# Kernel tuning notes

Hardware: AMD Instinct MI355X
Metric: run time of the kernel (lower is better)

The kernel has to match this reference:

```python
import jax, jax.numpy as jnp
import numpy as np

D = 512      # word_embedding_dim (dim_in == dim_out)
HEADS = 8    # isab_num_heads
M = 16       # isab_num_inds
B = 2048     # batch_news_num = batch_size * news_num
S = 32       # max_title_length
EPS = 1e-5   # torch LayerNorm default eps


def _layer_norm(x, g, b):
    mu = jnp.mean(x, axis=-1, keepdims=True)
    var = jnp.mean((x - mu) ** 2, axis=-1, keepdims=True)
    return (x - mu) * jax.lax.rsqrt(var + EPS) * g + b


def _mab(Qin, Kin, Wqkv, bqkv, Wo, bo, g0, b0, g1, b1):
    # Faithful to torch MAB: linear Q/K/V, head split via reshape (equivalent
    # to split/cat since cat-back restores head slices), scale by sqrt(dim_V).
    d = Wqkv.shape[-1]
    Q = Qin @ Wqkv[0] + bqkv[0]          # [B, Sq, d]
    K = Kin @ Wqkv[1] + bqkv[1]          # [B, Sk, d]
    V = Kin @ Wqkv[2] + bqkv[2]
    Bn, Sq, _ = Q.shape
    Sk = K.shape[1]
    hd = d // HEADS
    Qh = Q.reshape(Bn, Sq, HEADS, hd)
    Kh = K.reshape(Bn, Sk, HEADS, hd)
    Vh = V.reshape(Bn, Sk, HEADS, hd)
    scores = jnp.einsum('bqhd,bkhd->bhqk', Qh, Kh) / jnp.sqrt(jnp.asarray(d, Q.dtype))
    A = jax.nn.softmax(scores, axis=-1)
    Oh = Qh + jnp.einsum('bhqk,bkhd->bqhd', A, Vh)   # residual on Q_
    O = Oh.reshape(Bn, Sq, d)
    O = _layer_norm(O, g0, b0)                        # ln0
    O = O + jax.nn.relu(O @ Wo + bo)                  # O + relu(fc_o(O))
    O = _layer_norm(O, g1, b1)                        # ln1
    return O


def _isab(X, I, p0, p1):
    Iq = jnp.broadcast_to(I, (X.shape[0],) + I.shape[1:])  # I.repeat(B,1,1)
    Hm = _mab(Iq, X, *p0)   # mab0(I, X) -> [B, M, d]
    return _mab(X, Hm, *p1)  # mab1(X, H) -> [B, S, d]


def setup_inputs() -> dict:
    key = jax.random.key(0)
    ks = jax.random.split(key, 12)
    sc = 1.0 / np.sqrt(D)
    inp = {
        'x': jax.random.normal(ks[0], (B, S, D), dtype=jnp.float32),
        'I': jax.random.normal(ks[1], (1, M, D), dtype=jnp.float32) * sc,
        'mab0_Wqkv': jax.random.normal(ks[2], (3, D, D), dtype=jnp.float32) * sc,
        'mab0_bqkv': jnp.zeros((3, D), dtype=jnp.float32),
        'mab0_Wo': jax.random.normal(ks[3], (D, D), dtype=jnp.float32) * sc,
        'mab0_bo': jnp.zeros((D,), dtype=jnp.float32),
        'mab0_g0': jnp.ones((D,), dtype=jnp.float32),
        'mab0_b0': jnp.zeros((D,), dtype=jnp.float32),
        'mab0_g1': jnp.ones((D,), dtype=jnp.float32),
        'mab0_b1': jnp.zeros((D,), dtype=jnp.float32),
        'mab1_Wqkv': jax.random.normal(ks[4], (3, D, D), dtype=jnp.float32) * sc,
        'mab1_bqkv': jnp.zeros((3, D), dtype=jnp.float32),
        'mab1_Wo': jax.random.normal(ks[5], (D, D), dtype=jnp.float32) * sc,
        'mab1_bo': jnp.zeros((D,), dtype=jnp.float32),
        'mab1_g0': jnp.ones((D,), dtype=jnp.float32),
        'mab1_b0': jnp.zeros((D,), dtype=jnp.float32),
        'mab1_g1': jnp.ones((D,), dtype=jnp.float32),
        'mab1_b1': jnp.zeros((D,), dtype=jnp.float32),
    }
    return inp


def reference(x, I,
              mab0_Wqkv, mab0_bqkv, mab0_Wo, mab0_bo, mab0_g0, mab0_b0, mab0_g1, mab0_b1,
              mab1_Wqkv, mab1_bqkv, mab1_Wo, mab1_bo, mab1_g0, mab1_b0, mab1_g1, mab1_b1):
    p0 = (mab0_Wqkv, mab0_bqkv, mab0_Wo, mab0_bo, mab0_g0, mab0_b0, mab0_g1, mab0_b1)
    p1 = (mab1_Wqkv, mab1_bqkv, mab1_Wo, mab1_bo, mab1_g0, mab1_b0, mab1_g1, mab1_b1)
    # CIDER title path (eval mode, dropout=identity): ISAB applied twice, mean pool
    h1 = _isab(x, I, p0, p1)
    h2 = _isab(h1, I, p0, p1)
    return jnp.mean(h2, axis=1)   # [B, D] title_embedding
```

## Files before the change

kernel.cpp:

```cpp
#include <hip/hip_runtime.h>
#include <hip/hip_bf16.h>

#define D 512
#define BATCH 2048
#define SEQ 32
#define MIND 16

typedef __hip_bfloat16 bf16;
typedef __attribute__((ext_vector_type(8))) short s8v;
typedef __attribute__((ext_vector_type(4))) short s4v;
typedef __attribute__((ext_vector_type(4))) float f4v;

#define SWZ(row, kb) (((row) << 10) + ((kb) ^ (((row) & 7) << 4)))

__device__ __forceinline__ ushort f2bu(float f) {
    bf16 h = __float2bfloat16(f); ushort u; __builtin_memcpy(&u, &h, 2); return u;
}
__device__ __forceinline__ float bu2f(ushort u) {
    unsigned x = ((unsigned)u) << 16; float f; __builtin_memcpy(&f, &x, 4); return f;
}

__device__ __forceinline__ float wave_sum(float v) {
#pragma unroll
    for (int off = 32; off >= 1; off >>= 1) v += __shfl_xor(v, off, 64);
    return v;
}

struct WPtrs { const float* s[7]; };

__global__ __launch_bounds__(256) void wtrans7(WPtrs wp, ushort* __restrict__ Wt) {
    const float* W = wp.s[blockIdx.z];
    ushort* dst = Wt + (size_t)blockIdx.z * 262144;
    __shared__ float t[32][33];
    const int k0 = blockIdx.x * 32, n0 = blockIdx.y * 32;
    const int lx = threadIdx.x & 31, ly = threadIdx.x >> 5;
    for (int i = ly; i < 32; i += 8) t[i][lx] = W[(size_t)(k0 + i) * D + n0 + lx];
    __syncthreads();
    for (int i = ly; i < 32; i += 8)
        dst[(size_t)(n0 + i) * D + k0 + lx] = f2bu(t[lx][i]);
}

__global__ __launch_bounds__(256) void q0_kernel(
    const float* __restrict__ I, const float* __restrict__ Wq,
    const float* __restrict__ bq, ushort* __restrict__ Q0b)
{
    const int q = blockIdx.x;
    const int c = threadIdx.x;
    float a0 = 0.f, a1 = 0.f;
    for (int k = 0; k < D; ++k) {
        const float iv = I[q * D + k];
        a0 = fmaf(iv, Wq[(size_t)k * D + c], a0);
        a1 = fmaf(iv, Wq[(size_t)k * D + c + 256], a1);
    }
    Q0b[q * D + c]       = f2bu(a0 + bq[c]);
    Q0b[q * D + c + 256] = f2bu(a1 + bq[c + 256]);
}

__global__ __launch_bounds__(256) void conv_bf16(const float* __restrict__ x,
                                                 ushort* __restrict__ xb, long n4) {
    for (long i = (long)blockIdx.x * 256 + threadIdx.x; i < n4; i += (long)gridDim.x * 256) {
        const float4 v = ((const float4*)x)[i];
        s4v o = {(short)f2bu(v.x), (short)f2bu(v.y), (short)f2bu(v.z), (short)f2bu(v.w)};
        ((s4v*)xb)[i] = o;
    }
}

template <bool RESFUSE, bool LNA>
__global__ __launch_bounds__(512, 4) void gemm512(
    const ushort* __restrict__ Ab, const ushort* __restrict__ Wt,
    const float* __restrict__ bias,
    const float* __restrict__ lng, const float* __restrict__ lnb,
    ushort* __restrict__ Cb)
{
    __shared__ __align__(16) char sA[64 * 1024];
    const int tid = threadIdx.x, lane = tid & 63, wv = tid >> 6;
    const size_t m0 = (size_t)blockIdx.x * 64;

    for (int c = tid; c < 64 * 128; c += 512) {
        const int row = c >> 7, k4 = (c & 127) << 2;
        *(s4v*)(sA + SWZ(row, k4 * 2)) = *(const s4v*)(Ab + (m0 + row) * D + k4);
    }
    __syncthreads();

    if constexpr (LNA) {
        for (int i = wv; i < 64; i += 8) {
            float v[8];
#pragma unroll
            for (int j = 0; j < 8; ++j)
                v[j] = bu2f(*(const ushort*)(sA + SWZ(i, 2 * (lane + 64 * j))));
            float s = 0.f;
#pragma unroll
            for (int j = 0; j < 8; ++j) s += v[j];
            s = wave_sum(s);
            const float mu = s * (1.f / 512.f);
            float q2 = 0.f;
#pragma unroll
            for (int j = 0; j < 8; ++j) { const float t = v[j] - mu; q2 = fmaf(t, t, q2); }
            q2 = wave_sum(q2);
            const float inv = rsqrtf(q2 * (1.f / 512.f) + 1e-5f);
#pragma unroll
            for (int j = 0; j < 8; ++j) {
                const int d0 = lane + 64 * j;
                *(ushort*)(sA + SWZ(i, 2 * d0)) = f2bu((v[j] - mu) * inv * lng[d0] + lnb[d0]);
            }
        }
        __syncthreads();
    }

    constexpr int RT = 4;
    f4v acc[RT][4];
#pragma unroll
    for (int i = 0; i < RT; ++i)
#pragma unroll
        for (int j = 0; j < 4; ++j) acc[i][j] = (f4v){0.f, 0.f, 0.f, 0.f};
    const int m = lane & 15, g = lane >> 4;
    const int swm = (m & 7) << 4;
    const ushort* Bp = Wt + ((size_t)(wv * 64 + m) << 9) + 8 * g;

#pragma unroll
    for (int k0 = 0; k0 < 512; k0 += 32) {
        s8v bfr[4];
#pragma unroll
        for (int ct = 0; ct < 4; ++ct) bfr[ct] = *(const s8v*)(Bp + ct * 8192 + k0);
        const int kb = 2 * (k0 + 8 * g);
        s8v a[RT];
#pragma unroll
        for (int rt = 0; rt < RT; ++rt)
            a[rt] = *(const s8v*)(sA + ((rt * 16 + m) << 10) + (kb ^ swm));
#pragma unroll
        for (int ct = 0; ct < 4; ++ct)
#pragma unroll
            for (int rt = 0; rt < RT; ++rt)
                acc[rt][ct] = __builtin_amdgcn_mfma_f32_16x16x32_bf16(a[rt], bfr[ct], acc[rt][ct], 0, 0, 0);
    }

#pragma unroll
    for (int ct = 0; ct < 4; ++ct) {
        const int col = wv * 64 + ct * 16 + m;
        const float bb = bias[col];
#pragma unroll
        for (int rt = 0; rt < RT; ++rt)
#pragma unroll
            for (int r = 0; r < 4; ++r) {
                const int row = rt * 16 + g * 4 + r;
                float v = acc[rt][ct][r] + bb;
                if (RESFUSE)
                    v = bu2f(*(const ushort*)(sA + SWZ(row, 2 * col))) + fmaxf(v, 0.f);
                Cb[(m0 + row) * D + col] = f2bu(v);
            }
    }
}

template <int SQ, int SK, bool QSHARED>
__global__ __launch_bounds__(64) void attn_core(
    const ushort* __restrict__ Qb, const ushort* __restrict__ Kb,
    const ushort* __restrict__ Vb, ushort* __restrict__ Ob)
{
    constexpr int RS = 72;
    __shared__ __align__(16) ushort sQ[SQ * RS];
    __shared__ __align__(16) ushort sK[SK * RS];
    __shared__ __align__(16) ushort sV[SK * RS];
    __shared__ float sS[SQ][SK + 1];

    const int lane = threadIdx.x;
    const int b = blockIdx.x, h = blockIdx.y;
    const size_t qbase = (QSHARED ? (size_t)0 : (size_t)b * SQ * D) + h * 64;
    const size_t kbase = (size_t)b * SK * D + h * 64;

    for (int idx = lane; idx < SQ * 16; idx += 64) {
        const int r = idx >> 4, c4 = (idx & 15) << 2;
        *(s4v*)(sQ + r * RS + c4) = *(const s4v*)(Qb + qbase + (size_t)r * D + c4);
    }
    for (int idx = lane; idx < SK * 16; idx += 64) {
        const int r = idx >> 4, c4 = (idx & 15) << 2;
        *(s4v*)(sK + r * RS + c4) = *(const s4v*)(Kb + kbase + (size_t)r * D + c4);
        *(s4v*)(sV + r * RS + c4) = *(const s4v*)(Vb + kbase + (size_t)r * D + c4);
    }
    __syncthreads();

    const float scale = 0.044194173824159216f;
#pragma unroll
    for (int o = 0; o < SQ * SK / 64; ++o) {
        const int idx = o * 64 + lane;
        const int q = idx / SK, k = idx % SK;
        float s = 0.f;
#pragma unroll
        for (int dd = 0; dd < 64; dd += 8) {
            const s8v aq = *(const s8v*)(sQ + q * RS + dd);
            const s8v ak = *(const s8v*)(sK + k * RS + dd);
#pragma unroll
            for (int e = 0; e < 8; ++e)
                s = fmaf(bu2f((ushort)aq[e]), bu2f((ushort)ak[e]), s);
        }
        sS[q][k] = s * scale;
    }
    __syncthreads();

    if (lane < SQ) {
        float* row = sS[lane];
        float mx = row[0];
#pragma unroll
        for (int k = 1; k < SK; ++k) mx = fmaxf(mx, row[k]);
        float sum = 0.f;
#pragma unroll
        for (int k = 0; k < SK; ++k) { const float e = __expf(row[k] - mx); row[k] = e; sum += e; }
        const float inv = 1.f / sum;
#pragma unroll
        for (int k = 0; k < SK; ++k) row[k] *= inv;
    }
    __syncthreads();

    float acc[SQ];
#pragma unroll
    for (int q = 0; q < SQ; ++q) acc[q] = 0.f;
#pragma unroll 4
    for (int k = 0; k < SK; ++k) {
        const float v = bu2f(sV[k * RS + lane]);
#pragma unroll
        for (int q = 0; q < SQ; ++q) acc[q] = fmaf(sS[q][k], v, acc[q]);
    }
    const size_t obase = (size_t)b * SQ * D + h * 64 + lane;
#pragma unroll
    for (int q = 0; q < SQ; ++q)
        Ob[obase + (size_t)q * D] = f2bu(bu2f(sQ[q * RS + lane]) + acc[q]);
}

__global__ __launch_bounds__(512) void ln_meanpool(
    const ushort* __restrict__ U, const float* __restrict__ gg,
    const float* __restrict__ bb, float* __restrict__ outp)
{
    __shared__ float sP[8][512];
    const int tid = threadIdx.x, lane = tid & 63, wv = tid >> 6;
    const size_t b = blockIdx.x;
    float a[8];
#pragma unroll
    for (int j = 0; j < 8; ++j) a[j] = 0.f;
    for (int i = wv; i < 32; i += 8) {
        const ushort* u = U + ((size_t)b * 32 + i) * D;
        float v[8];
#pragma unroll
        for (int j = 0; j < 8; ++j) v[j] = bu2f(u[lane + 64 * j]);
        float s = 0.f;
#pragma unroll
        for (int j = 0; j < 8; ++j) s += v[j];
        s = wave_sum(s);
        const float mu = s * (1.f / 512.f);
        float q2 = 0.f;
#pragma unroll
        for (int j = 0; j < 8; ++j) { const float t = v[j] - mu; q2 = fmaf(t, t, q2); }
        q2 = wave_sum(q2);
        const float inv = rsqrtf(q2 * (1.f / 512.f) + 1e-5f);
#pragma unroll
        for (int j = 0; j < 8; ++j) {
            const int d0 = lane + 64 * j;
            a[j] += (v[j] - mu) * inv * gg[d0] + bb[d0];
        }
    }
#pragma unroll
    for (int j = 0; j < 8; ++j) sP[wv][lane + 64 * j] = a[j];
    __syncthreads();
    float s = 0.f;
#pragma unroll
    for (int w = 0; w < 8; ++w) s += sP[w][tid];
    outp[b * D + tid] = s * (1.f / 32.f);
}

extern "C" void kernel_launch(void* const* d_in, const int* in_sizes, int n_in,
                              void* d_out, int out_size, void* d_ws, size_t ws_size,
                              hipStream_t stream) {
    (void)in_sizes; (void)n_in; (void)out_size; (void)ws_size;

    const float* x     = (const float*)d_in[0];
    const float* I     = (const float*)d_in[1];
    const float* W0    = (const float*)d_in[2];
    const float* bqkv0 = (const float*)d_in[3];
    const float* Wo0   = (const float*)d_in[4];
    const float* bo0   = (const float*)d_in[5];
    const float* g00   = (const float*)d_in[6];
    const float* b00   = (const float*)d_in[7];
    const float* g01   = (const float*)d_in[8];
    const float* b01   = (const float*)d_in[9];
    const float* W1    = (const float*)d_in[10];
    const float* bqkv1 = (const float*)d_in[11];
    const float* Wo1   = (const float*)d_in[12];
    const float* bo1   = (const float*)d_in[13];
    const float* g10   = (const float*)d_in[14];
    const float* b10   = (const float*)d_in[15];
    const float* g11   = (const float*)d_in[16];
    const float* b11   = (const float*)d_in[17];

    const float* Wq0 = W0;     const float* Wk0 = W0 + D * D;  const float* Wv0 = W0 + 2 * D * D;
    const float* bq0 = bqkv0;  const float* bk0 = bqkv0 + D;   const float* bv0 = bqkv0 + 2 * D;
    const float* Wq1 = W1;     const float* Wk1 = W1 + D * D;  const float* Wv1 = W1 + 2 * D * D;
    const float* bq1 = bqkv1;  const float* bk1 = bqkv1 + D;   const float* bv1 = bqkv1 + 2 * D;

    char* ws = (char*)d_ws;
    ushort* Q0b = (ushort*)ws;
    ushort* Wt  = (ushort*)(ws + 32768);
    char* base = ws + 32768 + 7 * 524288;
    ushort* P0 = (ushort*)(base);
    ushort* P1 = (ushort*)(base + ((size_t)64 << 20));
    ushort* P2 = (ushort*)(base + ((size_t)128 << 20));
    ushort* P3 = (ushort*)(base + ((size_t)192 << 20));
    const size_t HALF = (size_t)16 << 20;
    ushort* P0hi = P0 + HALF;
    ushort* P1hi = P1 + HALF;
    ushort* P3hi = P3 + HALF;

    ushort* WtK0 = Wt + 0 * 262144;
    ushort* WtV0 = Wt + 1 * 262144;
    ushort* WtO0 = Wt + 2 * 262144;
    ushort* WtQ1 = Wt + 3 * 262144;
    ushort* WtK1 = Wt + 4 * 262144;
    ushort* WtV1 = Wt + 5 * 262144;
    ushort* WtO1 = Wt + 6 * 262144;

    WPtrs wp; wp.s[0] = Wk0; wp.s[1] = Wv0; wp.s[2] = Wo0; wp.s[3] = Wq1;
    wp.s[4] = Wk1; wp.s[5] = Wv1; wp.s[6] = Wo1;
    wtrans7<<<dim3(16, 16, 7), 256, 0, stream>>>(wp, Wt);
    q0_kernel<<<MIND, 256, 0, stream>>>(I, Wq0, bq0, Q0b);
    conv_bf16<<<4096, 256, 0, stream>>>(x, P0, (long)BATCH * SEQ * D / 4);

    constexpr int GBS = BATCH * SEQ / 64;
    constexpr int GBM = BATCH * MIND / 64;
    const dim3 ag(BATCH, 8);

    gemm512<false, false><<<GBS, 512, 0, stream>>>(P0, WtK0, bk0, g00, b00, P1);
    gemm512<false, false><<<GBS, 512, 0, stream>>>(P0, WtV0, bv0, g00, b00, P2);
    attn_core<MIND, SEQ, true><<<ag, 64, 0, stream>>>(Q0b, P1, P2, P3);
    gemm512<true, true><<<GBM, 512, 0, stream>>>(P3, WtO0, bo0, g00, b00, P3hi);
    gemm512<false, true><<<GBM, 512, 0, stream>>>(P3hi, WtK1, bk1, g01, b01, P1);
    gemm512<false, true><<<GBM, 512, 0, stream>>>(P3hi, WtV1, bv1, g01, b01, P1hi);
    gemm512<false, false><<<GBS, 512, 0, stream>>>(P0, WtQ1, bq1, g00, b00, P2);
    attn_core<SEQ, MIND, false><<<ag, 64, 0, stream>>>(P2, P1, P1hi, P0);
    gemm512<true, true><<<GBS, 512, 0, stream>>>(P0, WtO1, bo1, g10, b10, P3);

    gemm512<false, true><<<GBS, 512, 0, stream>>>(P3, WtK0, bk0, g11, b11, P1);
    gemm512<false, true><<<GBS, 512, 0, stream>>>(P3, WtV0, bv0, g11, b11, P2);
    attn_core<MIND, SEQ, true><<<ag, 64, 0, stream>>>(Q0b, P1, P2, P0);
    gemm512<true, true><<<GBM, 512, 0, stream>>>(P0, WtO0, bo0, g00, b00, P0hi);
    gemm512<false, true><<<GBM, 512, 0, stream>>>(P0hi, WtK1, bk1, g01, b01, P1);
    gemm512<false, true><<<GBM, 512, 0, stream>>>(P0hi, WtV1, bv1, g01, b01, P1hi);
    gemm512<false, true><<<GBS, 512, 0, stream>>>(P3, WtQ1, bq1, g11, b11, P2);
    attn_core<SEQ, MIND, false><<<ag, 64, 0, stream>>>(P2, P1, P1hi, P3);
    gemm512<true, true><<<GBS, 512, 0, stream>>>(P3, WtO1, bo1, g10, b10, P0);

    ln_meanpool<<<BATCH, 512, 0, stream>>>(P0, g11, b11, (float*)d_out);
}
```

Measured before the change: 1.502 ms.

## Fuse K/V/Q projections into one multi-output GEMM with staged coalesced stores

Replaces the single-output gemm512 with a templated gemmN that loads the A tile once and computes up to three projections (K, V, Q) against it, cutting repeated A loads and kernel launches. Epilogue results are staged through a swizzled shared buffer so global stores become 16-byte row writes instead of scattered 2-byte writes. The attention output is written in place with a strided layout, and a SPARSEA row remap lets the next GEMM read it directly, which shrinks the buffer set. The cost is extra shared memory and extra barriers in the epilogue, which may lower occupancy.

```diff
diff --git a/kernel.cpp b/kernel.cpp
--- a/kernel.cpp
+++ b/kernel.cpp
@@ -65,20 +65,24 @@
     }
 }
 
-template <bool RESFUSE, bool LNA>
-__global__ __launch_bounds__(512, 4) void gemm512(
-    const ushort* __restrict__ Ab, const ushort* __restrict__ Wt,
-    const float* __restrict__ bias,
-    const float* __restrict__ lng, const float* __restrict__ lnb,
-    ushort* __restrict__ Cb)
+template <int NOUT, bool RESFUSE, bool LNA, bool SPARSEA>
+__global__ __launch_bounds__(512, 4) void gemmN(
+    const ushort* __restrict__ Ab,
+    const ushort* __restrict__ Wt0, const float* __restrict__ bias0, ushort* __restrict__ C0,
+    const ushort* __restrict__ Wt1, const float* __restrict__ bias1, ushort* __restrict__ C1,
+    const ushort* __restrict__ Wt2, const float* __restrict__ bias2, ushort* __restrict__ C2,
+    const float* __restrict__ lng, const float* __restrict__ lnb)
 {
     __shared__ __align__(16) char sA[64 * 1024];
+    __shared__ __align__(16) char sC[16 * 1024];
     const int tid = threadIdx.x, lane = tid & 63, wv = tid >> 6;
     const size_t m0 = (size_t)blockIdx.x * 64;
 
-    for (int c = tid; c < 64 * 128; c += 512) {
-        const int row = c >> 7, k4 = (c & 127) << 2;
-        *(s4v*)(sA + SWZ(row, k4 * 2)) = *(const s4v*)(Ab + (m0 + row) * D + k4);
+    for (int c = tid; c < 64 * 64; c += 512) {
+        const int row = c >> 6, k8 = (c & 63) << 3;
+        const size_t L = m0 + row;
+        const size_t pr = SPARSEA ? ((L >> 4) * 32 + (L & 15)) : L;
+        *(s8v*)(sA + SWZ(row, k8 * 2)) = *(const s8v*)(Ab + pr * D + k8);
     }
     __syncthreads();
 
@@ -107,51 +111,67 @@
         __syncthreads();
     }
 
-    constexpr int RT = 4;
-    f4v acc[RT][4];
-#pragma unroll
-    for (int i = 0; i < RT; ++i)
-#pragma unroll
-        for (int j = 0; j < 4; ++j) acc[i][j] = (f4v){0.f, 0.f, 0.f, 0.f};
     const int m = lane & 15, g = lane >> 4;
     const int swm = (m & 7) << 4;
-    const ushort* Bp = Wt + ((size_t)(wv * 64 + m) << 9) + 8 * g;
-
-#pragma unroll
-    for (int k0 = 0; k0 < 512; k0 += 32) {
-        s8v bfr[4];
-#pragma unroll
-        for (int ct = 0; ct < 4; ++ct) bfr[ct] = *(const s8v*)(Bp + ct * 8192 + k0);
-        const int kb = 2 * (k0 + 8 * g);
-        s8v a[RT];
-#pragma unroll
-        for (int rt = 0; rt < RT; ++rt)
-            a[rt] = *(const s8v*)(sA + ((rt * 16 + m) << 10) + (kb ^ swm));
-#pragma unroll
-        for (int ct = 0; ct < 4; ++ct)
-#pragma unroll
-            for (int rt = 0; rt < RT; ++rt)
-                acc[rt][ct] = __builtin_amdgcn_mfma_f32_16x16x32_bf16(a[rt], bfr[ct], acc[rt][ct], 0, 0, 0);
-    }
-
-#pragma unroll
-    for (int ct = 0; ct < 4; ++ct) {
-        const int col = wv * 64 + ct * 16 + m;
-        const float bb = bias[col];
-#pragma unroll
-        for (int rt = 0; rt < RT; ++rt)
-#pragma unroll
-            for (int r = 0; r < 4; ++r) {
-                const int row = rt * 16 + g * 4 + r;
-                float v = acc[rt][ct][r] + bb;
-                if (RESFUSE)
-                    v = bu2f(*(const ushort*)(sA + SWZ(row, 2 * col))) + fmaxf(v, 0.f);
-                Cb[(m0 + row) * D + col] = f2bu(v);
+    const ushort* Wts[3]  = {Wt0, Wt1, Wt2};
+    const float*  bias[3] = {bias0, bias1, bias2};
+    ushort*       Cs[3]   = {C0, C1, C2};
+
+#pragma unroll
+    for (int o = 0; o < NOUT; ++o) {
+        const ushort* Bp = Wts[o] + ((size_t)(wv * 64 + m) << 9) + 8 * g;
+        f4v acc[4][4];
+#pragma unroll
+        for (int i = 0; i < 4; ++i)
+#pragma unroll
+            for (int j = 0; j < 4; ++j) acc[i][j] = (f4v){0.f, 0.f, 0.f, 0.f};
+
+#pragma unroll
+        for (int k0 = 0; k0 < 512; k0 += 32) {
+            s8v bfr[4];
+#pragma unroll
+            for (int ct = 0; ct < 4; ++ct) bfr[ct] = *(const s8v*)(Bp + ct * 8192 + k0);
+            const int kb = 2 * (k0 + 8 * g);
+            s8v a[4];
+#pragma unroll
+            for (int rt = 0; rt < 4; ++rt)
+                a[rt] = *(const s8v*)(sA + ((rt * 16 + m) << 10) + (kb ^ swm));
+#pragma unroll
+            for (int ct = 0; ct < 4; ++ct)
+#pragma unroll
+                for (int rt = 0; rt < 4; ++rt)
+                    acc[rt][ct] = __builtin_amdgcn_mfma_f32_16x16x32_bf16(a[rt], bfr[ct], acc[rt][ct], 0, 0, 0);
+        }
+
+        ushort* Cb = Cs[o];
+        const float* bb = bias[o];
+#pragma unroll 1
+        for (int rt = 0; rt < 4; ++rt) {
+            __syncthreads();
+#pragma unroll
+            for (int ct = 0; ct < 4; ++ct) {
+                const int col = wv * 64 + ct * 16 + m;
+                const float bv = bb[col];
+#pragma unroll
+                for (int r = 0; r < 4; ++r) {
+                    const int lrow = g * 4 + r;
+                    float v = acc[rt][ct][r] + bv;
+                    if (RESFUSE)
+                        v = bu2f(*(const ushort*)(sA + SWZ(rt * 16 + lrow, 2 * col))) + fmaxf(v, 0.f);
+                    *(ushort*)(sC + SWZ(lrow, 2 * col)) = f2bu(v);
+                }
             }
-    }
-}
-
-template <int SQ, int SK, bool QSHARED>
+            __syncthreads();
+            for (int c = tid; c < 16 * 64; c += 512) {
+                const int row = c >> 6, k8 = (c & 63) << 3;
+                *(s8v*)(Cb + (m0 + rt * 16 + row) * D + k8) = *(const s8v*)(sC + SWZ(row, k8 * 2));
+            }
+        }
+        __syncthreads();
+    }
+}
+
+template <int SQ, int SK, bool QSHARED, int OSTR>
 __global__ __launch_bounds__(64) void attn_core(
     const ushort* __restrict__ Qb, const ushort* __restrict__ Kb,
     const ushort* __restrict__ Vb, ushort* __restrict__ Ob)
@@ -219,7 +239,7 @@
 #pragma unroll
         for (int q = 0; q < SQ; ++q) acc[q] = fmaf(sS[q][k], v, acc[q]);
     }
-    const size_t obase = (size_t)b * SQ * D + h * 64 + lane;
+    const size_t obase = (size_t)b * OSTR * D + h * 64 + lane;
 #pragma unroll
     for (int q = 0; q < SQ; ++q)
         Ob[obase + (size_t)q * D] = f2bu(bu2f(sQ[q * RS + lane]) + acc[q]);
@@ -302,10 +322,8 @@
     ushort* P1 = (ushort*)(base + ((size_t)64 << 20));
     ushort* P2 = (ushort*)(base + ((size_t)128 << 20));
     ushort* P3 = (ushort*)(base + ((size_t)192 << 20));
-    const size_t HALF = (size_t)16 << 20;
-    ushort* P0hi = P0 + HALF;
-    ushort* P1hi = P1 + HALF;
-    ushort* P3hi = P3 + HALF;
+    const size_t HALFE = (size_t)16 << 20;
+    ushort* P1hi = P1 + HALFE;
 
     ushort* WtK0 = Wt + 0 * 262144;
     ushort* WtV0 = Wt + 1 * 262144;
@@ -325,25 +343,22 @@
     constexpr int GBM = BATCH * MIND / 64;
     const dim3 ag(BATCH, 8);
 
-    gemm512<false, false><<<GBS, 512, 0, stream>>>(P0, WtK0, bk0, g00, b00, P1);
-    gemm512<false, false><<<GBS, 512, 0, stream>>>(P0, WtV0, bv0, g00, b00, P2);
-    attn_core<MIND, SEQ, true><<<ag, 64, 0, stream>>>(Q0b, P1, P2, P3);
-    gemm512<true, true><<<GBM, 512, 0, stream>>>(P3, WtO0, bo0, g00, b00, P3hi);
-    gemm512<false, true><<<GBM, 512, 0, stream>>>(P3hi, WtK1, bk1, g01, b01, P1);
-    gemm512<false, true><<<GBM, 512, 0, stream>>>(P3hi, WtV1, bv1, g01, b01, P1hi);
-    gemm512<false, false><<<GBS, 512, 0, stream>>>(P0, WtQ1, bq1, g00, b00, P2);
-    attn_core<SEQ, MIND, false><<<ag, 64, 0, stream>>>(P2, P1, P1hi, P0);
-    gemm512<true, true><<<GBS, 512, 0, stream>>>(P0, WtO1, bo1, g10, b10, P3);
-
-    gemm512<false, true><<<GBS, 512, 0, stream>>>(P3, WtK0, bk0, g11, b11, P1);
-    gemm512<false, true><<<GBS, 512, 0, stream>>>(P3, WtV0, bv0, g11, b11, P2);
-    attn_core<MIND, SEQ, true><<<ag, 64, 0, stream>>>(Q0b, P1, P2, P0);
-    gemm512<true, true><<<GBM, 512, 0, stream>>>(P0, WtO0, bo0, g00, b00, P0hi);
-    gemm512<false, true><<<GBM, 512, 0, stream>>>(P0hi, WtK1, bk1, g01, b01, P1);
-    gemm512<false, true><<<GBM, 512, 0, stream>>>(P0hi, WtV1, bv1, g01, b01, P1hi);
-    gemm512<false, true><<<GBS, 512, 0, stream>>>(P3, WtQ1, bq1, g11, b11, P2);
-    attn_core<SEQ, MIND, false><<<ag, 64, 0, stream>>>(P2, P1, P1hi, P3);
-    gemm512<true, true><<<GBS, 512, 0, stream>>>(P3, WtO1, bo1, g10, b10, P0);
+    for (int isab = 0; isab < 2; ++isab) {
+        if (isab == 0)
+            gemmN<3, false, false, false><<<GBS, 512, 0, stream>>>(
+                P0, WtK0, bk0, P1, WtV0, bv0, P2, WtQ1, bq1, P3, nullptr, nullptr);
+        else
+            gemmN<3, false, true, false><<<GBS, 512, 0, stream>>>(
+                P0, WtK0, bk0, P1, WtV0, bv0, P2, WtQ1, bq1, P3, g11, b11);
+        attn_core<MIND, SEQ, true, 32><<<ag, 64, 0, stream>>>(Q0b, P1, P2, P1);
+        gemmN<1, true, true, true><<<GBM, 512, 0, stream>>>(
+            P1, WtO0, bo0, P2, nullptr, nullptr, nullptr, nullptr, nullptr, nullptr, g00, b00);
+        gemmN<2, false, true, false><<<GBM, 512, 0, stream>>>(
+            P2, WtK1, bk1, P1, WtV1, bv1, P1hi, nullptr, nullptr, nullptr, g01, b01);
+        attn_core<SEQ, MIND, false, 32><<<ag, 64, 0, stream>>>(P3, P1, P1hi, P3);
+        gemmN<1, true, true, false><<<GBS, 512, 0, stream>>>(
+            P3, WtO1, bo1, P0, nullptr, nullptr, nullptr, nullptr, nullptr, nullptr, g10, b10);
+    }
 
     ln_meanpool<<<BATCH, 512, 0, stream>>>(P0, g11, b11, (float*)d_out);
 }
```

After: 4.363 ms. 191% more time.
